# Optimization experiments

Measured on AMD Instinct MI355X. Metric: run time of the kernel, lower is better.

The kernel has to match this reference:

```python
import jax, jax.numpy as jnp
import numpy as np

N_NODES = 50000
N_EDGES = 800000
D = 64


def setup_inputs() -> dict:
    key = jax.random.key(0)
    ks = jax.random.split(key, 8)
    scale = 1.0 / np.sqrt(D)
    x = jax.random.normal(ks[0], (N_NODES, D), dtype=jnp.float32)
    edge_index = jax.random.randint(ks[1], (2, N_EDGES), 0, N_NODES, dtype=jnp.int64)
    W1_root = jax.random.normal(ks[2], (D, D), dtype=jnp.float32) * scale
    W1_nbr = jax.random.normal(ks[3], (D, D), dtype=jnp.float32) * scale
    b1 = jnp.zeros((D,), dtype=jnp.float32)
    W2_root = jax.random.normal(ks[4], (D, D), dtype=jnp.float32) * scale
    W2_nbr = jax.random.normal(ks[5], (D, D), dtype=jnp.float32) * scale
    b2 = jnp.zeros((D,), dtype=jnp.float32)
    return {"x": x, "edge_index": edge_index,
            "W1_root": W1_root, "W1_nbr": W1_nbr, "b1": b1,
            "W2_root": W2_root, "W2_nbr": W2_nbr, "b2": b2}


def graph_conv(x, src, dst, W_root, W_nbr, b, n_nodes):
    # sum-aggregate neighbor features: msg j->i uses x[src], scattered to dst
    agg = jax.ops.segment_sum(x[src], dst, num_segments=n_nodes)  # [N, D]
    return x @ W_root + agg @ W_nbr + b


def reference(x, edge_index, W1_root, W1_nbr, b1, W2_root, W2_nbr, b2):
    src, dst = edge_index[0], edge_index[1]
    n = x.shape[0]
    h = jax.nn.relu(graph_conv(x, src, dst, W1_root, W1_nbr, b1, n))
    out = graph_conv(h, src, dst, W2_root, W2_nbr, b2, n)
    return out
```

## Files before the change

kernel.cpp:

```cpp
#include <hip/hip_runtime.h>

#define N_NODES 50000
#define N_EDGES 800000
#define D 64
#define NBUCKETS 782
#define NPB 64
#define BCAP 2048
#define SBLOCKS 256
#define CHUNK (N_EDGES / SBLOCKS)
#define MB ((N_NODES + 63) / 64)

typedef short bf16x8 __attribute__((ext_vector_type(8)));
typedef float f32x4  __attribute__((ext_vector_type(4)));

__device__ __forceinline__ unsigned short f2bf(float f) {
    unsigned u = __float_as_uint(f);
    return (unsigned short)((u + 0x7fffu + ((u >> 16) & 1u)) >> 16);
}
__device__ __forceinline__ float bflo(unsigned u) {
    return __uint_as_float(u << 16);
}
__device__ __forceinline__ float bfhi(unsigned u) {
    return __uint_as_float(u & 0xffff0000u);
}

__global__ void __launch_bounds__(256) prep_kernel(
    const float* __restrict__ W1r, const float* __restrict__ W1n,
    const float* __restrict__ W2r, const float* __restrict__ W2n,
    int* __restrict__ cursorPad, unsigned short* __restrict__ wt) {
    int t = threadIdx.x;
    if (blockIdx.x == 4) {
        for (int i = t; i < NBUCKETS * 16; i += 256) cursorPad[i] = 0;
        return;
    }
    const float* Wsrc = blockIdx.x == 0 ? W1r : blockIdx.x == 1 ? W1n
                      : blockIdx.x == 2 ? W2r : W2n;
    unsigned short* dstw = wt + blockIdx.x * D * D;
    for (int i = t; i < D * D; i += 256) {
        int k = i >> 6, c = i & 63;
        dstw[c * D + k] = f2bf(Wsrc[i]);
    }
}

__device__ __forceinline__ void scatter_body(
    const int* __restrict__ src, const int* __restrict__ dst,
    int* __restrict__ cursorPad, int* __restrict__ staged,
    char* smem, int bid, int t) {
    int* hist = (int*)smem;
    int* curs = (int*)(smem + 3200);
    int* pk   = (int*)(smem + 6400);
    unsigned short* bk = (unsigned short*)(smem + 6400 + 12500);
    for (int i = t; i < NBUCKETS; i += 256) hist[i] = 0;
    __syncthreads();
    int lo = bid * CHUNK;
    for (int i = t; i < CHUNK; i += 256) {
        int d = dst[lo + i];
        int s = src[lo + i];
        pk[i] = (s << 6) | (d & 63);
        bk[i] = (unsigned short)(d >> 6);
        atomicAdd(&hist[d >> 6], 1);
    }
    __syncthreads();
    for (int k = t; k < NBUCKETS; k += 256)
        if (hist[k] > 0)
            curs[k] = k * BCAP + atomicAdd(&cursorPad[k * 16], hist[k]);
    __syncthreads();
    for (int i = t; i < CHUNK; i += 256) {
        int b = bk[i];
        int pos = atomicAdd(&curs[b], 1);
        staged[pos] = pk[i];
    }
}

template<int XBF>
__device__ __forceinline__ void gemm_mfma_body(
    const float* __restrict__ Xf, const unsigned short* __restrict__ Xb,
    const unsigned short* __restrict__ Wtr, const unsigned short* __restrict__ Wtn,
    float* __restrict__ outR, unsigned short* __restrict__ outN,
    int node0, int tid) {
    int wave = tid >> 6, lane = tid & 63;
    int rbase = node0 + wave * 16;
    int rrow  = lane & 15;
    int kg    = lane >> 4;
    int row   = min(rbase + rrow, N_NODES - 1);

    bf16x8 a0, a1;
    if (XBF) {
        a0 = *(const bf16x8*)(Xb + (size_t)row * D + kg * 8);
        a1 = *(const bf16x8*)(Xb + (size_t)row * D + 32 + kg * 8);
    } else {
        const float* xp = Xf + (size_t)row * D + kg * 8;
#pragma unroll
        for (int j = 0; j < 8; j++) a0[j] = (short)f2bf(xp[j]);
#pragma unroll
        for (int j = 0; j < 8; j++) a1[j] = (short)f2bf(xp[32 + j]);
    }

    f32x4 accR[4], accN[4];
#pragma unroll
    for (int t = 0; t < 4; t++) {
        accR[t][0] = 0.f; accR[t][1] = 0.f; accR[t][2] = 0.f; accR[t][3] = 0.f;
        accN[t][0] = 0.f; accN[t][1] = 0.f; accN[t][2] = 0.f; accN[t][3] = 0.f;
    }

#pragma unroll
    for (int t = 0; t < 4; t++) {
        int c = t * 16 + rrow;
        bf16x8 br0 = *(const bf16x8*)(Wtr + c * D + kg * 8);
        bf16x8 br1 = *(const bf16x8*)(Wtr + c * D + 32 + kg * 8);
        bf16x8 bn0 = *(const bf16x8*)(Wtn + c * D + kg * 8);
        bf16x8 bn1 = *(const bf16x8*)(Wtn + c * D + 32 + kg * 8);
        accR[t] = __builtin_amdgcn_mfma_f32_16x16x32_bf16(a0, br0, accR[t], 0, 0, 0);
        accR[t] = __builtin_amdgcn_mfma_f32_16x16x32_bf16(a1, br1, accR[t], 0, 0, 0);
        accN[t] = __builtin_amdgcn_mfma_f32_16x16x32_bf16(a0, bn0, accN[t], 0, 0, 0);
        accN[t] = __builtin_amdgcn_mfma_f32_16x16x32_bf16(a1, bn1, accN[t], 0, 0, 0);
    }

#pragma unroll
    for (int t = 0; t < 4; t++) {
#pragma unroll
        for (int i = 0; i < 4; i++) {
            int n = rbase + kg * 4 + i;
            if (n < N_NODES) {
                int c = t * 16 + rrow;
                outR[(size_t)n * D + c] = accR[t][i];
                outN[(size_t)n * D + c] = f2bf(accN[t][i]);
            }
        }
    }
}

__global__ void __launch_bounds__(256) scatter_gemm1(
    const int* __restrict__ src, const int* __restrict__ dst,
    int* __restrict__ cursorPad, int* __restrict__ staged,
    const float* __restrict__ X, const unsigned short* __restrict__ wt,
    float* __restrict__ xr, unsigned short* __restrict__ xn) {
    __shared__ char smem[25600];
    if (blockIdx.x < SBLOCKS) {
        scatter_body(src, dst, cursorPad, staged, smem, blockIdx.x, threadIdx.x);
    } else {
        gemm_mfma_body<0>(X, (const unsigned short*)0,
                          wt + 0 * D * D, wt + 1 * D * D,
                          xr, xn, (blockIdx.x - SBLOCKS) * 64, threadIdx.x);
    }
}

__global__ void __launch_bounds__(256) gemm2(
    const unsigned short* __restrict__ Xb, const unsigned short* __restrict__ wt,
    float* __restrict__ hr, unsigned short* __restrict__ hn) {
    gemm_mfma_body<1>((const float*)0, Xb,
                      wt + 2 * D * D, wt + 3 * D * D,
                      hr, hn, blockIdx.x * 64, threadIdx.x);
}

__global__ void __launch_bounds__(256) csr_build_kernel(
    const int* __restrict__ cursorPad, const int* __restrict__ staged,
    int* __restrict__ csr, int* __restrict__ startEnd) {
    __shared__ int deg[NPB];
    __shared__ int sc[NPB];
    __shared__ int curs[NPB];
    __shared__ int lcsr[BCAP];
    int k = blockIdx.x;
    int t = threadIdx.x;
    int base = k * BCAP;
    int cnt  = cursorPad[k * 16];
    if (t < NPB) deg[t] = 0;
    __syncthreads();
    for (int i = t; i < cnt; i += 256)
        atomicAdd(&deg[staged[base + i] & 63], 1);
    __syncthreads();
    int v = (t < NPB) ? deg[t] : 0;
    if (t < NPB) sc[t] = v;
    __syncthreads();
#pragma unroll
    for (int d = 1; d < NPB; d <<= 1) {
        int u = (t < NPB && t >= d) ? sc[t - d] : 0;
        __syncthreads();
        if (t < NPB) sc[t] += u;
        __syncthreads();
    }
    if (t < NPB) {
        int start = sc[t] - v;
        int node = k * NPB + t;
        if (node < N_NODES) {
            int2 se; se.x = base + start; se.y = base + start + v;
            ((int2*)startEnd)[node] = se;
        }
        curs[t] = start;
    }
    __syncthreads();
    for (int i = t; i < cnt; i += 256) {
        int e = staged[base + i];
        int pos = atomicAdd(&curs[e & 63], 1);
        lcsr[pos] = e >> 6;
    }
    __syncthreads();
    for (int i = t; i < cnt; i += 256)
        csr[base + i] = lcsr[i];
}

template<int RELU, int OUTBF>
__global__ void __launch_bounds__(256) gather_fused(
    const unsigned short* __restrict__ Gsrc, const float* __restrict__ Root,
    const float* __restrict__ bias,
    const int* __restrict__ startEnd, const int* __restrict__ csr,
    float* __restrict__ outF, unsigned short* __restrict__ outB) {
    int tid = threadIdx.x;
    int wave = tid >> 6, lane = tid & 63;
    int nA = blockIdx.x * 8 + wave * 2;
    int nB = nA + 1;
    int sub = lane >> 3, fq = lane & 7;

    int4 se = *(const int4*)(startEnd + nA * 2);
    int jbA = se.x, jeA = se.y, jbB = se.z, jeB = se.w;

    float4 xA0, xA1, xB0, xB1, b0, b1;
    if (sub == 0) {
        const float* rpA = Root + (size_t)nA * D + fq * 8;
        const float* rpB = Root + (size_t)nB * D + fq * 8;
        xA0 = *(const float4*)rpA; xA1 = *(const float4*)(rpA + 4);
        xB0 = *(const float4*)rpB; xB1 = *(const float4*)(rpB + 4);
        b0 = ((const float4*)bias)[fq * 2];
        b1 = ((const float4*)bias)[fq * 2 + 1];
    }

    float aA0=0.f,aA1=0.f,aA2=0.f,aA3=0.f,aA4=0.f,aA5=0.f,aA6=0.f,aA7=0.f;
    float aB0=0.f,aB1=0.f,aB2=0.f,aB3=0.f,aB4=0.f,aB5=0.f,aB6=0.f,aB7=0.f;

    while (jbA < jeA || jbB < jeB) {
        int pA = 0, pB = 0, mA = 0, mB = 0;
        if (jbA < jeA) {
            int idx = jbA + lane;
            pA = csr[idx < jeA ? idx : (jeA - 1)];
            mA = min(64, jeA - jbA);
        }
        if (jbB < jeB) {
            int idx = jbB + lane;
            pB = csr[idx < jeB ? idx : (jeB - 1)];
            mB = min(64, jeB - jbB);
        }
        if (mA) {
            int b = 0;
            for (; b + 16 <= mA; b += 16) {
                int i0 = __shfl(pA, b + sub, 64);
                int i1 = __shfl(pA, b + 8 + sub, 64);
                uint4 u0 = *(const uint4*)(Gsrc + i0 * D + fq * 8);
                uint4 u1 = *(const uint4*)(Gsrc + i1 * D + fq * 8);
                aA0 += bflo(u0.x) + bflo(u1.x);  aA1 += bfhi(u0.x) + bfhi(u1.x);
                aA2 += bflo(u0.y) + bflo(u1.y);  aA3 += bfhi(u0.y) + bfhi(u1.y);
                aA4 += bflo(u0.z) + bflo(u1.z);  aA5 += bfhi(u0.z) + bfhi(u1.z);
                aA6 += bflo(u0.w) + bflo(u1.w);  aA7 += bfhi(u0.w) + bfhi(u1.w);
            }
            for (; b < mA; b += 8) {
                int sidx = b + sub;
                int scl = sidx < mA ? sidx : (mA - 1);
                int i0 = __shfl(pA, scl, 64);
                if (sidx < mA) {
                    uint4 u = *(const uint4*)(Gsrc + i0 * D + fq * 8);
                    aA0 += bflo(u.x); aA1 += bfhi(u.x);
                    aA2 += bflo(u.y); aA3 += bfhi(u.y);
                    aA4 += bflo(u.z); aA5 += bfhi(u.z);
                    aA6 += bflo(u.w); aA7 += bfhi(u.w);
                }
            }
        }
        if (mB) {
            int b = 0;
            for (; b + 16 <= mB; b += 16) {
                int i0 = __shfl(pB, b + sub, 64);
                int i1 = __shfl(pB, b + 8 + sub, 64);
                uint4 u0 = *(const uint4*)(Gsrc + i0 * D + fq * 8);
                uint4 u1 = *(const uint4*)(Gsrc + i1 * D + fq * 8);
                aB0 += bflo(u0.x) + bflo(u1.x);  aB1 += bfhi(u0.x) + bfhi(u1.x);
                aB2 += bflo(u0.y) + bflo(u1.y);  aB3 += bfhi(u0.y) + bfhi(u1.y);
                aB4 += bflo(u0.z) + bflo(u1.z);  aB5 += bfhi(u0.z) + bfhi(u1.z);
                aB6 += bflo(u0.w) + bflo(u1.w);  aB7 += bfhi(u0.w) + bfhi(u1.w);
            }
            for (; b < mB; b += 8) {
                int sidx = b + sub;
                int scl = sidx < mB ? sidx : (mB - 1);
                int i0 = __shfl(pB, scl, 64);
                if (sidx < mB) {
                    uint4 u = *(const uint4*)(Gsrc + i0 * D + fq * 8);
                    aB0 += bflo(u.x); aB1 += bfhi(u.x);
                    aB2 += bflo(u.y); aB3 += bfhi(u.y);
                    aB4 += bflo(u.z); aB5 += bfhi(u.z);
                    aB6 += bflo(u.w); aB7 += bfhi(u.w);
                }
            }
        }
        jbA += 64; jbB += 64;
    }

#pragma unroll
    for (int mk = 8; mk <= 32; mk <<= 1) {
        aA0 += __shfl_xor(aA0, mk, 64); aA1 += __shfl_xor(aA1, mk, 64);
        aA2 += __shfl_xor(aA2, mk, 64); aA3 += __shfl_xor(aA3, mk, 64);
        aA4 += __shfl_xor(aA4, mk, 64); aA5 += __shfl_xor(aA5, mk, 64);
        aA6 += __shfl_xor(aA6, mk, 64); aA7 += __shfl_xor(aA7, mk, 64);
        aB0 += __shfl_xor(aB0, mk, 64); aB1 += __shfl_xor(aB1, mk, 64);
        aB2 += __shfl_xor(aB2, mk, 64); aB3 += __shfl_xor(aB3, mk, 64);
        aB4 += __shfl_xor(aB4, mk, 64); aB5 += __shfl_xor(aB5, mk, 64);
        aB6 += __shfl_xor(aB6, mk, 64); aB7 += __shfl_xor(aB7, mk, 64);
    }
    if (sub == 0) {
        float r0 = aA0 + xA0.x + b0.x, r1 = aA1 + xA0.y + b0.y;
        float r2 = aA2 + xA0.z + b0.z, r3 = aA3 + xA0.w + b0.w;
        float r4 = aA4 + xA1.x + b1.x, r5 = aA5 + xA1.y + b1.y;
        float r6 = aA6 + xA1.z + b1.z, r7 = aA7 + xA1.w + b1.w;
        float s0 = aB0 + xB0.x + b0.x, s1 = aB1 + xB0.y + b0.y;
        float s2 = aB2 + xB0.z + b0.z, s3 = aB3 + xB0.w + b0.w;
        float s4 = aB4 + xB1.x + b1.x, s5 = aB5 + xB1.y + b1.y;
        float s6 = aB6 + xB1.z + b1.z, s7 = aB7 + xB1.w + b1.w;
        if (RELU) {
            r0 = fmaxf(r0, 0.f); r1 = fmaxf(r1, 0.f);
            r2 = fmaxf(r2, 0.f); r3 = fmaxf(r3, 0.f);
            r4 = fmaxf(r4, 0.f); r5 = fmaxf(r5, 0.f);
            r6 = fmaxf(r6, 0.f); r7 = fmaxf(r7, 0.f);
            s0 = fmaxf(s0, 0.f); s1 = fmaxf(s1, 0.f);
            s2 = fmaxf(s2, 0.f); s3 = fmaxf(s3, 0.f);
            s4 = fmaxf(s4, 0.f); s5 = fmaxf(s5, 0.f);
            s6 = fmaxf(s6, 0.f); s7 = fmaxf(s7, 0.f);
        }
        if (OUTBF) {
            uint4 u;
            u.x = (unsigned)f2bf(r0) | ((unsigned)f2bf(r1) << 16);
            u.y = (unsigned)f2bf(r2) | ((unsigned)f2bf(r3) << 16);
            u.z = (unsigned)f2bf(r4) | ((unsigned)f2bf(r5) << 16);
            u.w = (unsigned)f2bf(r6) | ((unsigned)f2bf(r7) << 16);
            *(uint4*)(outB + (size_t)nA * D + fq * 8) = u;
            u.x = (unsigned)f2bf(s0) | ((unsigned)f2bf(s1) << 16);
            u.y = (unsigned)f2bf(s2) | ((unsigned)f2bf(s3) << 16);
            u.z = (unsigned)f2bf(s4) | ((unsigned)f2bf(s5) << 16);
            u.w = (unsigned)f2bf(s6) | ((unsigned)f2bf(s7) << 16);
            *(uint4*)(outB + (size_t)nB * D + fq * 8) = u;
        } else {
            float4 w0; w0.x = r0; w0.y = r1; w0.z = r2; w0.w = r3;
            float4 w1; w1.x = r4; w1.y = r5; w1.z = r6; w1.w = r7;
            *(float4*)(outF + (size_t)nA * D + fq * 8) = w0;
            *(float4*)(outF + (size_t)nA * D + fq * 8 + 4) = w1;
            w0.x = s0; w0.y = s1; w0.z = s2; w0.w = s3;
            w1.x = s4; w1.y = s5; w1.z = s6; w1.w = s7;
            *(float4*)(outF + (size_t)nB * D + fq * 8) = w0;
            *(float4*)(outF + (size_t)nB * D + fq * 8 + 4) = w1;
        }
    }
}

extern "C" void kernel_launch(void* const* d_in, const int* in_sizes, int n_in,
                              void* d_out, int out_size, void* d_ws, size_t ws_size,
                              hipStream_t stream) {
    const float* x   = (const float*)d_in[0];
    const int*   edg = (const int*)d_in[1];
    const float* W1r = (const float*)d_in[2];
    const float* W1n = (const float*)d_in[3];
    const float* b1  = (const float*)d_in[4];
    const float* W2r = (const float*)d_in[5];
    const float* W2n = (const float*)d_in[6];
    const float* b2  = (const float*)d_in[7];
    float* out = (float*)d_out;

    const int* src = edg;
    const int* dst = edg + N_EDGES;

    int* W              = (int*)d_ws;
    int* cursorPad      = W;
    int* staged         = W + NBUCKETS * 16;
    int* csr            = staged + NBUCKETS * BCAP;
    int* startEnd       = csr + NBUCKETS * BCAP;
    float* xr           = (float*)(startEnd + 2 * N_NODES);
    unsigned short* xn  = (unsigned short*)(xr + (size_t)N_NODES * D);
    unsigned short* hbf = xn + (size_t)N_NODES * D;
    float* hr           = (float*)(hbf + (size_t)N_NODES * D);
    unsigned short* hn  = (unsigned short*)(hr + (size_t)N_NODES * D);
    unsigned short* wt  = hn + (size_t)N_NODES * D;

    prep_kernel<<<5, 256, 0, stream>>>(W1r, W1n, W2r, W2n, cursorPad, wt);

    scatter_gemm1<<<SBLOCKS + MB, 256, 0, stream>>>(
        src, dst, cursorPad, staged, x, wt, xr, xn);

    csr_build_kernel<<<NBUCKETS, 256, 0, stream>>>(cursorPad, staged, csr,
                                                   startEnd);

    const int GB2 = N_NODES / 8;

    gather_fused<1, 1><<<GB2, 256, 0, stream>>>(
        xn, xr, b1, startEnd, csr, (float*)0, hbf);

    gemm2<<<MB, 256, 0, stream>>>(hbf, wt, hr, hn);

    gather_fused<0, 0><<<GB2, 256, 0, stream>>>(
        hn, hr, b2, startEnd, csr, out, (unsigned short*)0);
}
```

Before: 172.3 us.

## Fuse layer-1 gather with layer-2 GEMM through LDS tile

The layer-1 gather kernel now runs 512-thread blocks covering 16 nodes. It writes the ReLU'd bf16 rows of h into a small LDS tile and immediately runs MFMA against W2_root and W2_nbr to produce hr and hn. This removes the separate gemm2 launch and the global round trip of the h buffer. In exchange, each block does a tiny 16-row GEMM with weights read from global memory, and the larger blocks with a barrier may lower gather occupancy.

```diff
diff --git a/kernel.cpp b/kernel.cpp
--- a/kernel.cpp
+++ b/kernel.cpp
@@ -145,14 +145,6 @@
     }
 }
 
-__global__ void __launch_bounds__(256) gemm2(
-    const unsigned short* __restrict__ Xb, const unsigned short* __restrict__ wt,
-    float* __restrict__ hr, unsigned short* __restrict__ hn) {
-    gemm_mfma_body<1>((const float*)0, Xb,
-                      wt + 2 * D * D, wt + 3 * D * D,
-                      hr, hn, blockIdx.x * 64, threadIdx.x);
-}
-
 __global__ void __launch_bounds__(256) csr_build_kernel(
     const int* __restrict__ cursorPad, const int* __restrict__ staged,
     int* __restrict__ csr, int* __restrict__ startEnd) {
@@ -199,15 +191,17 @@
         csr[base + i] = lcsr[i];
 }
 
-template<int RELU, int OUTBF>
-__global__ void __launch_bounds__(256) gather_fused(
+__global__ void __launch_bounds__(512) gather1_gemm2(
     const unsigned short* __restrict__ Gsrc, const float* __restrict__ Root,
     const float* __restrict__ bias,
     const int* __restrict__ startEnd, const int* __restrict__ csr,
-    float* __restrict__ outF, unsigned short* __restrict__ outB) {
+    const unsigned short* __restrict__ wt,
+    float* __restrict__ hr, unsigned short* __restrict__ hn) {
+    __shared__ unsigned short hlds[16][72];
     int tid = threadIdx.x;
     int wave = tid >> 6, lane = tid & 63;
-    int nA = blockIdx.x * 8 + wave * 2;
+    int n0 = blockIdx.x * 16;
+    int nA = n0 + wave * 2;
     int nB = nA + 1;
     int sub = lane >> 3, fq = lane & 7;
 
@@ -304,46 +298,170 @@
         aB6 += __shfl_xor(aB6, mk, 64); aB7 += __shfl_xor(aB7, mk, 64);
     }
     if (sub == 0) {
-        float r0 = aA0 + xA0.x + b0.x, r1 = aA1 + xA0.y + b0.y;
-        float r2 = aA2 + xA0.z + b0.z, r3 = aA3 + xA0.w + b0.w;
-        float r4 = aA4 + xA1.x + b1.x, r5 = aA5 + xA1.y + b1.y;
-        float r6 = aA6 + xA1.z + b1.z, r7 = aA7 + xA1.w + b1.w;
-        float s0 = aB0 + xB0.x + b0.x, s1 = aB1 + xB0.y + b0.y;
-        float s2 = aB2 + xB0.z + b0.z, s3 = aB3 + xB0.w + b0.w;
-        float s4 = aB4 + xB1.x + b1.x, s5 = aB5 + xB1.y + b1.y;
-        float s6 = aB6 + xB1.z + b1.z, s7 = aB7 + xB1.w + b1.w;
-        if (RELU) {
-            r0 = fmaxf(r0, 0.f); r1 = fmaxf(r1, 0.f);
-            r2 = fmaxf(r2, 0.f); r3 = fmaxf(r3, 0.f);
-            r4 = fmaxf(r4, 0.f); r5 = fmaxf(r5, 0.f);
-            r6 = fmaxf(r6, 0.f); r7 = fmaxf(r7, 0.f);
-            s0 = fmaxf(s0, 0.f); s1 = fmaxf(s1, 0.f);
-            s2 = fmaxf(s2, 0.f); s3 = fmaxf(s3, 0.f);
-            s4 = fmaxf(s4, 0.f); s5 = fmaxf(s5, 0.f);
-            s6 = fmaxf(s6, 0.f); s7 = fmaxf(s7, 0.f);
-        }
-        if (OUTBF) {
-            uint4 u;
-            u.x = (unsigned)f2bf(r0) | ((unsigned)f2bf(r1) << 16);
-            u.y = (unsigned)f2bf(r2) | ((unsigned)f2bf(r3) << 16);
-            u.z = (unsigned)f2bf(r4) | ((unsigned)f2bf(r5) << 16);
-            u.w = (unsigned)f2bf(r6) | ((unsigned)f2bf(r7) << 16);
-            *(uint4*)(outB + (size_t)nA * D + fq * 8) = u;
-            u.x = (unsigned)f2bf(s0) | ((unsigned)f2bf(s1) << 16);
-            u.y = (unsigned)f2bf(s2) | ((unsigned)f2bf(s3) << 16);
-            u.z = (unsigned)f2bf(s4) | ((unsigned)f2bf(s5) << 16);
-            u.w = (unsigned)f2bf(s6) | ((unsigned)f2bf(s7) << 16);
-            *(uint4*)(outB + (size_t)nB * D + fq * 8) = u;
-        } else {
-            float4 w0; w0.x = r0; w0.y = r1; w0.z = r2; w0.w = r3;
-            float4 w1; w1.x = r4; w1.y = r5; w1.z = r6; w1.w = r7;
-            *(float4*)(outF + (size_t)nA * D + fq * 8) = w0;
-            *(float4*)(outF + (size_t)nA * D + fq * 8 + 4) = w1;
-            w0.x = s0; w0.y = s1; w0.z = s2; w0.w = s3;
-            w1.x = s4; w1.y = s5; w1.z = s6; w1.w = s7;
-            *(float4*)(outF + (size_t)nB * D + fq * 8) = w0;
-            *(float4*)(outF + (size_t)nB * D + fq * 8 + 4) = w1;
-        }
+        float r0 = fmaxf(aA0 + xA0.x + b0.x, 0.f), r1 = fmaxf(aA1 + xA0.y + b0.y, 0.f);
+        float r2 = fmaxf(aA2 + xA0.z + b0.z, 0.f), r3 = fmaxf(aA3 + xA0.w + b0.w, 0.f);
+        float r4 = fmaxf(aA4 + xA1.x + b1.x, 0.f), r5 = fmaxf(aA5 + xA1.y + b1.y, 0.f);
+        float r6 = fmaxf(aA6 + xA1.z + b1.z, 0.f), r7 = fmaxf(aA7 + xA1.w + b1.w, 0.f);
+        float s0 = fmaxf(aB0 + xB0.x + b0.x, 0.f), s1 = fmaxf(aB1 + xB0.y + b0.y, 0.f);
+        float s2 = fmaxf(aB2 + xB0.z + b0.z, 0.f), s3 = fmaxf(aB3 + xB0.w + b0.w, 0.f);
+        float s4 = fmaxf(aB4 + xB1.x + b1.x, 0.f), s5 = fmaxf(aB5 + xB1.y + b1.y, 0.f);
+        float s6 = fmaxf(aB6 + xB1.z + b1.z, 0.f), s7 = fmaxf(aB7 + xB1.w + b1.w, 0.f);
+        uint4 u;
+        u.x = (unsigned)f2bf(r0) | ((unsigned)f2bf(r1) << 16);
+        u.y = (unsigned)f2bf(r2) | ((unsigned)f2bf(r3) << 16);
+        u.z = (unsigned)f2bf(r4) | ((unsigned)f2bf(r5) << 16);
+        u.w = (unsigned)f2bf(r6) | ((unsigned)f2bf(r7) << 16);
+        *(uint4*)&hlds[wave * 2][fq * 8] = u;
+        u.x = (unsigned)f2bf(s0) | ((unsigned)f2bf(s1) << 16);
+        u.y = (unsigned)f2bf(s2) | ((unsigned)f2bf(s3) << 16);
+        u.z = (unsigned)f2bf(s4) | ((unsigned)f2bf(s5) << 16);
+        u.w = (unsigned)f2bf(s6) | ((unsigned)f2bf(s7) << 16);
+        *(uint4*)&hlds[wave * 2 + 1][fq * 8] = u;
+    }
+    __syncthreads();
+
+    int t4   = wave >> 1;
+    int kind = wave & 1;
+    int rrow = lane & 15;
+    int kg   = lane >> 4;
+    bf16x8 a0 = *(const bf16x8*)&hlds[rrow][kg * 8];
+    bf16x8 a1 = *(const bf16x8*)&hlds[rrow][32 + kg * 8];
+    const unsigned short* Wt = wt + (2 + kind) * D * D;
+    int c = t4 * 16 + rrow;
+    bf16x8 bw0 = *(const bf16x8*)(Wt + c * D + kg * 8);
+    bf16x8 bw1 = *(const bf16x8*)(Wt + c * D + 32 + kg * 8);
+    f32x4 acc;
+    acc[0] = 0.f; acc[1] = 0.f; acc[2] = 0.f; acc[3] = 0.f;
+    acc = __builtin_amdgcn_mfma_f32_16x16x32_bf16(a0, bw0, acc, 0, 0, 0);
+    acc = __builtin_amdgcn_mfma_f32_16x16x32_bf16(a1, bw1, acc, 0, 0, 0);
+    if (kind == 0) {
+#pragma unroll
+        for (int i = 0; i < 4; i++)
+            hr[(size_t)(n0 + kg * 4 + i) * D + c] = acc[i];
+    } else {
+#pragma unroll
+        for (int i = 0; i < 4; i++)
+            hn[(size_t)(n0 + kg * 4 + i) * D + c] = f2bf(acc[i]);
+    }
+}
+
+__global__ void __launch_bounds__(256) gather2_out(
+    const unsigned short* __restrict__ Gsrc, const float* __restrict__ Root,
+    const float* __restrict__ bias,
+    const int* __restrict__ startEnd, const int* __restrict__ csr,
+    float* __restrict__ outF) {
+    int tid = threadIdx.x;
+    int wave = tid >> 6, lane = tid & 63;
+    int nA = blockIdx.x * 8 + wave * 2;
+    int nB = nA + 1;
+    int sub = lane >> 3, fq = lane & 7;
+
+    int4 se = *(const int4*)(startEnd + nA * 2);
+    int jbA = se.x, jeA = se.y, jbB = se.z, jeB = se.w;
+
+    float4 xA0, xA1, xB0, xB1, b0, b1;
+    if (sub == 0) {
+        const float* rpA = Root + (size_t)nA * D + fq * 8;
+        const float* rpB = Root + (size_t)nB * D + fq * 8;
+        xA0 = *(const float4*)rpA; xA1 = *(const float4*)(rpA + 4);
+        xB0 = *(const float4*)rpB; xB1 = *(const float4*)(rpB + 4);
+        b0 = ((const float4*)bias)[fq * 2];
+        b1 = ((const float4*)bias)[fq * 2 + 1];
+    }
+
+    float aA0=0.f,aA1=0.f,aA2=0.f,aA3=0.f,aA4=0.f,aA5=0.f,aA6=0.f,aA7=0.f;
+    float aB0=0.f,aB1=0.f,aB2=0.f,aB3=0.f,aB4=0.f,aB5=0.f,aB6=0.f,aB7=0.f;
+
+    while (jbA < jeA || jbB < jeB) {
+        int pA = 0, pB = 0, mA = 0, mB = 0;
+        if (jbA < jeA) {
+            int idx = jbA + lane;
+            pA = csr[idx < jeA ? idx : (jeA - 1)];
+            mA = min(64, jeA - jbA);
+        }
+        if (jbB < jeB) {
+            int idx = jbB + lane;
+            pB = csr[idx < jeB ? idx : (jeB - 1)];
+            mB = min(64, jeB - jbB);
+        }
+        if (mA) {
+            int b = 0;
+            for (; b + 16 <= mA; b += 16) {
+                int i0 = __shfl(pA, b + sub, 64);
+                int i1 = __shfl(pA, b + 8 + sub, 64);
+                uint4 u0 = *(const uint4*)(Gsrc + i0 * D + fq * 8);
+                uint4 u1 = *(const uint4*)(Gsrc + i1 * D + fq * 8);
+                aA0 += bflo(u0.x) + bflo(u1.x);  aA1 += bfhi(u0.x) + bfhi(u1.x);
+                aA2 += bflo(u0.y) + bflo(u1.y);  aA3 += bfhi(u0.y) + bfhi(u1.y);
+                aA4 += bflo(u0.z) + bflo(u1.z);  aA5 += bfhi(u0.z) + bfhi(u1.z);
+                aA6 += bflo(u0.w) + bflo(u1.w);  aA7 += bfhi(u0.w) + bfhi(u1.w);
+            }
+            for (; b < mA; b += 8) {
+                int sidx = b + sub;
+                int scl = sidx < mA ? sidx : (mA - 1);
+                int i0 = __shfl(pA, scl, 64);
+                if (sidx < mA) {
+                    uint4 u = *(const uint4*)(Gsrc + i0 * D + fq * 8);
+                    aA0 += bflo(u.x); aA1 += bfhi(u.x);
+                    aA2 += bflo(u.y); aA3 += bfhi(u.y);
+                    aA4 += bflo(u.z); aA5 += bfhi(u.z);
+                    aA6 += bflo(u.w); aA7 += bfhi(u.w);
+                }
+            }
+        }
+        if (mB) {
+            int b = 0;
+            for (; b + 16 <= mB; b += 16) {
+                int i0 = __shfl(pB, b + sub, 64);
+                int i1 = __shfl(pB, b + 8 + sub, 64);
+                uint4 u0 = *(const uint4*)(Gsrc + i0 * D + fq * 8);
+                uint4 u1 = *(const uint4*)(Gsrc + i1 * D + fq * 8);
+                aB0 += bflo(u0.x) + bflo(u1.x);  aB1 += bfhi(u0.x) + bfhi(u1.x);
+                aB2 += bflo(u0.y) + bflo(u1.y);  aB3 += bfhi(u0.y) + bfhi(u1.y);
+                aB4 += bflo(u0.z) + bflo(u1.z);  aB5 += bfhi(u0.z) + bfhi(u1.z);
+                aB6 += bflo(u0.w) + bflo(u1.w);  aB7 += bfhi(u0.w) + bfhi(u1.w);
+            }
+            for (; b < mB; b += 8) {
+                int sidx = b + sub;
+                int scl = sidx < mB ? sidx : (mB - 1);
+                int i0 = __shfl(pB, scl, 64);
+                if (sidx < mB) {
+                    uint4 u = *(const uint4*)(Gsrc + i0 * D + fq * 8);
+                    aB0 += bflo(u.x); aB1 += bfhi(u.x);
+                    aB2 += bflo(u.y); aB3 += bfhi(u.y);
+                    aB4 += bflo(u.z); aB5 += bfhi(u.z);
+                    aB6 += bflo(u.w); aB7 += bfhi(u.w);
+                }
+            }
+        }
+        jbA += 64; jbB += 64;
+    }
+
+#pragma unroll
+    for (int mk = 8; mk <= 32; mk <<= 1) {
+        aA0 += __shfl_xor(aA0, mk, 64); aA1 += __shfl_xor(aA1, mk, 64);
+        aA2 += __shfl_xor(aA2, mk, 64); aA3 += __shfl_xor(aA3, mk, 64);
+        aA4 += __shfl_xor(aA4, mk, 64); aA5 += __shfl_xor(aA5, mk, 64);
+        aA6 += __shfl_xor(aA6, mk, 64); aA7 += __shfl_xor(aA7, mk, 64);
+        aB0 += __shfl_xor(aB0, mk, 64); aB1 += __shfl_xor(aB1, mk, 64);
+        aB2 += __shfl_xor(aB2, mk, 64); aB3 += __shfl_xor(aB3, mk, 64);
+        aB4 += __shfl_xor(aB4, mk, 64); aB5 += __shfl_xor(aB5, mk, 64);
+        aB6 += __shfl_xor(aB6, mk, 64); aB7 += __shfl_xor(aB7, mk, 64);
+    }
+    if (sub == 0) {
+        float4 w0, w1;
+        w0.x = aA0 + xA0.x + b0.x; w0.y = aA1 + xA0.y + b0.y;
+        w0.z = aA2 + xA0.z + b0.z; w0.w = aA3 + xA0.w + b0.w;
+        w1.x = aA4 + xA1.x + b1.x; w1.y = aA5 + xA1.y + b1.y;
+        w1.z = aA6 + xA1.z + b1.z; w1.w = aA7 + xA1.w + b1.w;
+        *(float4*)(outF + (size_t)nA * D + fq * 8) = w0;
+        *(float4*)(outF + (size_t)nA * D + fq * 8 + 4) = w1;
+        w0.x = aB0 + xB0.x + b0.x; w0.y = aB1 + xB0.y + b0.y;
+        w0.z = aB2 + xB0.z + b0.z; w0.w = aB3 + xB0.w + b0.w;
+        w1.x = aB4 + xB1.x + b1.x; w1.y = aB5 + xB1.y + b1.y;
+        w1.z = aB6 + xB1.z + b1.z; w1.w = aB7 + xB1.w + b1.w;
+        *(float4*)(outF + (size_t)nB * D + fq * 8) = w0;
+        *(float4*)(outF + (size_t)nB * D + fq * 8 + 4) = w1;
     }
 }
 
@@ -370,8 +488,7 @@
     int* startEnd       = csr + NBUCKETS * BCAP;
     float* xr           = (float*)(startEnd + 2 * N_NODES);
     unsigned short* xn  = (unsigned short*)(xr + (size_t)N_NODES * D);
-    unsigned short* hbf = xn + (size_t)N_NODES * D;
-    float* hr           = (float*)(hbf + (size_t)N_NODES * D);
+    float* hr           = (float*)(xn + (size_t)N_NODES * D);
     unsigned short* hn  = (unsigned short*)(hr + (size_t)N_NODES * D);
     unsigned short* wt  = hn + (size_t)N_NODES * D;
 
@@ -383,13 +500,9 @@
     csr_build_kernel<<<NBUCKETS, 256, 0, stream>>>(cursorPad, staged, csr,
                                                    startEnd);
 
-    const int GB2 = N_NODES / 8;
-
-    gather_fused<1, 1><<<GB2, 256, 0, stream>>>(
-        xn, xr, b1, startEnd, csr, (float*)0, hbf);
-
-    gemm2<<<MB, 256, 0, stream>>>(hbf, wt, hr, hn);
-
-    gather_fused<0, 0><<<GB2, 256, 0, stream>>>(
-        hn, hr, b2, startEnd, csr, out, (unsigned short*)0);
-}
+    gather1_gemm2<<<N_NODES / 16, 512, 0, stream>>>(
+        xn, xr, b1, startEnd, csr, wt, hr, hn);
+
+    gather2_out<<<N_NODES / 8, 256, 0, stream>>>(
+        hn, hr, b2, startEnd, csr, out);
+}
```

New measurement: 168.3 us, median of 2. -2.3%, faster.
